# Performance work log

Hardware: AMD Instinct MI355X
Metric: run time of the kernel (lower is better)

## Reference

```python
import jax, jax.numpy as jnp
import numpy as np

B, NQ, NK = 4, 2048, 2048
D_MODEL, H, DK, DV, M = 512, 8, 64, 64, 40


def setup_inputs() -> dict:
    key = jax.random.key(0)
    ks = jax.random.split(key, 12)
    s = 0.02  # param init scale (stand-in for xavier)
    return {
        "queries": jax.random.normal(ks[0], (B, NQ, D_MODEL), jnp.float32),
        "keys": jax.random.normal(ks[1], (B, NK, D_MODEL), jnp.float32),
        "values": jax.random.normal(ks[2], (B, NK, D_MODEL), jnp.float32),
        "attention_weights": jax.random.uniform(ks[3], (B, H, NQ, NK), jnp.float32),
        "attention_mask": jax.random.randint(ks[4], (B, H, NQ, NK), 0, 2) == 1,
        "Wq": jax.random.normal(ks[5], (D_MODEL, H * DK), jnp.float32) * s,
        "bq": jnp.zeros((H * DK,), jnp.float32),
        "Wk": jax.random.normal(ks[6], (D_MODEL, H * DK), jnp.float32) * s,
        "bk": jnp.zeros((H * DK,), jnp.float32),
        "Wv": jax.random.normal(ks[7], (D_MODEL, H * DV), jnp.float32) * s,
        "bv": jnp.zeros((H * DV,), jnp.float32),
        "Wo": jax.random.normal(ks[8], (H * DV, D_MODEL), jnp.float32) * s,
        "bo": jnp.zeros((D_MODEL,), jnp.float32),
        "m_k": jax.random.normal(ks[9], (1, M, H * DK), jnp.float32) * s,
        "m_v": jax.random.normal(ks[10], (1, M, H * DV), jnp.float32) * s,
    }


def reference(queries, keys, values, attention_weights, attention_mask,
              Wq, bq, Wk, bk, Wv, bv, Wo, bo, m_k, m_v):
    b, nq, _ = queries.shape
    nk = keys.shape[1]
    # learned memory slots, scaled and broadcast over batch
    mk = jnp.sqrt(jnp.float32(DK)) * jnp.broadcast_to(m_k, (b, M, H * DK))
    mv = jnp.sqrt(jnp.float32(M)) * jnp.broadcast_to(m_v, (b, M, H * DV))
    q = (queries @ Wq + bq).reshape(b, nq, H, DK).transpose(0, 2, 1, 3)      # (b,h,nq,dk)
    k = jnp.concatenate([keys @ Wk + bk, mk], axis=1)
    k = k.reshape(b, nk + M, H, DK).transpose(0, 2, 3, 1)                     # (b,h,dk,nk+m)
    v = jnp.concatenate([values @ Wv + bv, mv], axis=1)
    v = v.reshape(b, nk + M, H, DV).transpose(0, 2, 1, 3)                     # (b,h,nk+m,dv)
    att = jnp.matmul(q, k) / jnp.sqrt(jnp.float32(DK))                        # (b,h,nq,nk+m)
    att_x = att[..., :nk] * attention_weights
    att_x = jnp.where(attention_mask, -jnp.inf, att_x)
    att = jnp.concatenate([att_x, att[..., nk:]], axis=-1)
    att = jax.nn.softmax(att, axis=-1)
    out = jnp.matmul(att, v).transpose(0, 2, 1, 3).reshape(b, nq, H * DV)
    return out @ Wo + bo
```

## Files before the change

kernel.cpp:

```cpp
#include <hip/hip_runtime.h>
#include <hip/hip_bf16.h>
#include <cstdint>
#include <cstddef>

typedef __bf16 bf16_t;
typedef __bf16 bf16x8 __attribute__((ext_vector_type(8)));
typedef __bf16 bf16x4 __attribute__((ext_vector_type(4)));
typedef float  f32x4  __attribute__((ext_vector_type(4)));

#define B_    4
#define NQ_   2048
#define NK_   2048
#define H_    8
#define MSL_  40
#define NKP_  2112
#define SCL2  0.18033688011112042f

#define GLOAD_LDS16(GP, LP)                                                        \
    __builtin_amdgcn_global_load_lds(                                              \
        (const __attribute__((address_space(1))) unsigned int*)(GP),               \
        (__attribute__((address_space(3))) unsigned int*)(LP), 16, 0, 0)

__global__ void detect_mask(const unsigned int* __restrict__ m, int* __restrict__ flag)
{
    __shared__ int found;
    if (threadIdx.x == 0) found = 0;
    __syncthreads();
    unsigned int acc = 0;
    for (int i = threadIdx.x; i < 65536; i += 256)
        acc |= (m[i] & 0xFFFFFF00u);
    if (acc) found = 1;
    __syncthreads();
    if (threadIdx.x == 0) *flag = found;
}

__global__ void transpose_convert4(const float* __restrict__ s0, const float* __restrict__ s1,
                                   const float* __restrict__ s2, const float* __restrict__ s3,
                                   bf16_t* __restrict__ d0, bf16_t* __restrict__ d1,
                                   bf16_t* __restrict__ d2, bf16_t* __restrict__ d3)
{
    const float* src; bf16_t* dst;
    switch (blockIdx.z) {
        case 0:  src = s0; dst = d0; break;
        case 1:  src = s1; dst = d1; break;
        case 2:  src = s2; dst = d2; break;
        default: src = s3; dst = d3; break;
    }
    __shared__ float t[32][33];
    int x  = blockIdx.x * 32 + threadIdx.x;
    int y0 = blockIdx.y * 32 + threadIdx.y;
#pragma unroll
    for (int i = 0; i < 32; i += 8)
        t[threadIdx.y + i][threadIdx.x] = src[(size_t)(y0 + i) * 512 + x];
    __syncthreads();
    int ox  = blockIdx.y * 32 + threadIdx.x;
    int oy0 = blockIdx.x * 32 + threadIdx.y;
#pragma unroll
    for (int i = 0; i < 32; i += 8)
        dst[(size_t)(oy0 + i) * 512 + ox] = (bf16_t)t[threadIdx.x][threadIdx.y + i];
}

__global__ void memfill(const float* __restrict__ m_k, const float* __restrict__ m_v,
                        bf16_t* __restrict__ Kbf, bf16_t* __restrict__ Vt)
{
    int tid = blockIdx.x * 256 + threadIdx.x;
    if (tid < 4 * 64 * 512) {
        int c  = tid & 511;
        int mi = (tid >> 9) & 63;
        int b  = tid >> 15;
        float v = (mi < MSL_) ? 8.0f * m_k[mi * 512 + c] : 0.0f;
        Kbf[((size_t)b * NKP_ + NK_ + mi) * 512 + c] = (bf16_t)v;
    } else {
        int t  = tid - 4 * 64 * 512;
        int mi = t & 63;
        int dv = (t >> 6) & 63;
        int h  = (t >> 12) & 7;
        int b  = t >> 15;
        float v = (mi < MSL_) ? 6.324555320336759f * m_v[mi * 512 + h * 64 + dv] : 0.0f;
        Vt[(((size_t)b * H_ + h) * 64 + dv) * NKP_ + NK_ + mi] = (bf16_t)v;
    }
}

template<bool AF32>
__device__ __forceinline__ void gemm_core(
    bf16_t (*As)[72], bf16_t (*Bs)[72],
    const void* __restrict__ Av, const bf16_t* __restrict__ BT,
    const float* __restrict__ bias, void* __restrict__ dstv,
    int dstBS, int epi, float scale)
{
    const int tid = threadIdx.x;
    const int w = tid >> 6, l = tid & 63, lg = l >> 4, lr = l & 15;
    const int wr = w >> 1, wc = w & 1;
    const int blockM = blockIdx.x * 128, blockN = blockIdx.y * 128;

    f32x4 acc[4][4];
    const f32x4 zv = {0.f, 0.f, 0.f, 0.f};
#pragma unroll
    for (int i = 0; i < 4; i++)
#pragma unroll
        for (int j = 0; j < 4; j++) acc[i][j] = zv;

    const int ar = tid >> 1;
    const int ac = (tid & 1) * 32;

    for (int k0 = 0; k0 < 512; k0 += 64) {
        if (k0) __syncthreads();
        if constexpr (AF32) {
            const float* arow = (const float*)Av + (size_t)(blockM + ar) * 512 + k0 + ac;
#pragma unroll
            for (int i = 0; i < 8; i++) {
                float4 v = ((const float4*)arow)[i];
                bf16x4 pk = {(bf16_t)v.x, (bf16_t)v.y, (bf16_t)v.z, (bf16_t)v.w};
                *(bf16x4*)&As[ar][ac + i * 4] = pk;
            }
        } else {
            const bf16_t* arow = (const bf16_t*)Av + (size_t)(blockM + ar) * 512 + k0 + ac;
#pragma unroll
            for (int i = 0; i < 4; i++)
                *(uint4*)&As[ar][ac + i * 8] = ((const uint4*)arow)[i];
        }
        {
            const bf16_t* brow = BT + (size_t)(blockN + ar) * 512 + k0 + ac;
#pragma unroll
            for (int i = 0; i < 4; i++)
                *(uint4*)&Bs[ar][ac + i * 8] = ((const uint4*)brow)[i];
        }
        __syncthreads();
#pragma unroll
        for (int ks = 0; ks < 2; ks++) {
            bf16x8 af[4], bfr[4];
#pragma unroll
            for (int mi = 0; mi < 4; mi++)
                af[mi] = *(const bf16x8*)&As[wr * 64 + mi * 16 + lr][ks * 32 + lg * 8];
#pragma unroll
            for (int ni = 0; ni < 4; ni++)
                bfr[ni] = *(const bf16x8*)&Bs[wc * 64 + ni * 16 + lr][ks * 32 + lg * 8];
#pragma unroll
            for (int mi = 0; mi < 4; mi++)
#pragma unroll
                for (int ni = 0; ni < 4; ni++)
                    acc[mi][ni] = __builtin_amdgcn_mfma_f32_16x16x32_bf16(af[mi], bfr[ni], acc[mi][ni], 0, 0, 0);
        }
    }

    const int colbase = blockN + wc * 64;
    float bias_v[4];
#pragma unroll
    for (int ni = 0; ni < 4; ni++) bias_v[ni] = bias[colbase + ni * 16 + lr];

#pragma unroll
    for (int mi = 0; mi < 4; mi++) {
        const int r0 = blockM + wr * 64 + mi * 16 + lg * 4;
#pragma unroll
        for (int ni = 0; ni < 4; ni++) {
            const int c = colbase + ni * 16 + lr;
            f32x4 v = acc[mi][ni];
            if (epi == 2) {
                float* dst = (float*)dstv;
#pragma unroll
                for (int j = 0; j < 4; j++)
                    dst[(size_t)(r0 + j) * 512 + c] = (v[j] + bias_v[ni]) * scale;
            } else if (epi == 0) {
                bf16_t* dst = (bf16_t*)dstv;
#pragma unroll
                for (int j = 0; j < 4; j++) {
                    int rr = r0 + j;
                    int bb = rr >> 11, nn = rr & 2047;
                    dst[((size_t)bb * dstBS + nn) * 512 + c] = (bf16_t)((v[j] + bias_v[ni]) * scale);
                }
            } else {
                bf16_t* dst = (bf16_t*)dstv;
                int bb = r0 >> 11, n0 = r0 & 2047;
                int hh = c >> 6, dv = c & 63;
                bf16x4 pk;
#pragma unroll
                for (int j = 0; j < 4; j++) pk[j] = (bf16_t)((v[j] + bias_v[ni]) * scale);
                *(bf16x4*)(dst + (((size_t)bb * H_ + hh) * 64 + dv) * NKP_ + n0) = pk;
            }
        }
    }
}

__global__ __launch_bounds__(256) void gemm_qkv(
    const float* __restrict__ q, const float* __restrict__ k, const float* __restrict__ v,
    const bf16_t* __restrict__ WqT, const bf16_t* __restrict__ WkT, const bf16_t* __restrict__ WvT,
    const float* __restrict__ bq, const float* __restrict__ bk, const float* __restrict__ bv,
    bf16_t* __restrict__ Qbf, bf16_t* __restrict__ Kbf, bf16_t* __restrict__ Vt)
{
    __shared__ bf16_t As[128][72];
    __shared__ bf16_t Bs[128][72];
    const void* Av; const bf16_t* BT; const float* bias; void* dst;
    int dstBS, epi; float scale = 1.0f;
    switch (blockIdx.z) {
        case 0:  Av = q; BT = WqT; bias = bq; dst = Qbf; dstBS = 2048; epi = 0; scale = SCL2; break;
        case 1:  Av = k; BT = WkT; bias = bk; dst = Kbf; dstBS = NKP_; epi = 0; break;
        default: Av = v; BT = WvT; bias = bv; dst = Vt;  dstBS = 0;    epi = 1; break;
    }
    gemm_core<true>(As, Bs, Av, BT, bias, dst, dstBS, epi, scale);
}

__global__ __launch_bounds__(256) void gemm_fin(
    const bf16_t* __restrict__ Obuf, const bf16_t* __restrict__ WoT,
    const float* __restrict__ bo, float* __restrict__ out)
{
    __shared__ bf16_t As[128][72];
    __shared__ bf16_t Bs[128][72];
    gemm_core<false>(As, Bs, Obuf, WoT, bo, out, 0, 2, 1.0f);
}

template<bool BYTEM>
__global__ __launch_bounds__(512) void attn_fused(
    const bf16_t* __restrict__ Qbf, const bf16_t* __restrict__ Kbf,
    const bf16_t* __restrict__ Vt, const float* __restrict__ attw,
    const void* __restrict__ maskv, const int* __restrict__ mflag,
    bf16_t* __restrict__ Obuf)
{
    if ((*mflag != 0) != BYTEM) return;

    __shared__ bf16_t Ks[2][64][64];
    __shared__ bf16_t Vs[2][64][64];
    __shared__ bf16_t Pl[8][1024];

    const int tid = threadIdx.x;
    const int wv = tid >> 6, l = tid & 63, lg = l >> 4, lr = l & 15;
    const int qt = blockIdx.x, h = blockIdx.y, b = blockIdx.z;
    const int q0w = qt * 128 + wv * 16;
    bf16_t* Pw = &Pl[wv][0];

    const size_t bh = (size_t)(b * H_ + h);
    const float* wbase = attw + bh * (size_t)NQ_ * NK_;
    const unsigned char* mb8 = (const unsigned char*)maskv + bh * (size_t)NQ_ * NK_;
    const int* mb32 = (const int*)maskv + bh * (size_t)NQ_ * NK_;
    const char* kbase8 = (const char*)(Kbf + (size_t)b * NKP_ * 512 + h * 64);
    const char* vbase8 = (const char*)(Vt + bh * 64 * (size_t)NKP_);

    bf16x8 qf0 = *(const bf16x8*)&Qbf[((size_t)b * NQ_ + q0w + lr) * 512 + h * 64 + lg * 8];
    bf16x8 qf1 = *(const bf16x8*)&Qbf[((size_t)b * NQ_ + q0w + lr) * 512 + h * 64 + 32 + lg * 8];

    const f32x4 zv = {0.f, 0.f, 0.f, 0.f};
    f32x4 oacc[4];
#pragma unroll
    for (int i = 0; i < 4; i++) oacc[i] = zv;
    float lsum = 0.f;
    f32x4 sA[4];

    f32x4 wA[4], wB[4];
    unsigned mA[4], mB[4];
    unsigned miA[16], miB[16];

    const int srow = l >> 3;
    const int scsw = ((l & 7) ^ (srow & 7)) * 16;

#define STAGE(BUF, KCB) do {                                                      \
    const int r_ = wv * 8 + srow;                                                 \
    GLOAD_LDS16(kbase8 + (size_t)((KCB) + r_) * 1024 + scsw,                      \
                (char*)&Ks[BUF][0][0] + wv * 1024);                               \
    GLOAD_LDS16(vbase8 + (size_t)r_ * 4224 + (size_t)(KCB) * 2 + scsw,            \
                (char*)&Vs[BUF][0][0] + wv * 1024);                               \
} while (0)

#define PREFETCH(KT, WB_, MB_, MIB_) do {                                         \
    const float* wp_ = wbase + (size_t)(q0w + lr) * NK_ + (KT) * 64 + lg * 4;     \
    _Pragma("unroll") for (int n_ = 0; n_ < 4; n_++)                              \
        WB_[n_] = *(const f32x4*)(wp_ + n_ * 16);                                 \
    if constexpr (BYTEM) {                                                        \
        const unsigned char* mp_ = mb8 + (size_t)(q0w + lr) * NK_ + (KT) * 64 + lg * 4; \
        _Pragma("unroll") for (int n_ = 0; n_ < 4; n_++)                          \
            MB_[n_] = *(const unsigned*)(mp_ + n_ * 16);                          \
    } else {                                                                      \
        const int* mp_ = mb32 + (size_t)(q0w + lr) * NK_ + (KT) * 64 + lg * 4;    \
        _Pragma("unroll") for (int n_ = 0; n_ < 4; n_++) {                        \
            uint4 t_ = *(const uint4*)(mp_ + n_ * 16);                            \
            MIB_[n_ * 4 + 0] = t_.x; MIB_[n_ * 4 + 1] = t_.y;                     \
            MIB_[n_ * 4 + 2] = t_.z; MIB_[n_ * 4 + 3] = t_.w; }                   \
    }                                                                             \
} while (0)

#define QKT_LDS(BC) do {                                                          \
    const int sw_ = (lg ^ (lr & 7)) * 8;                                          \
    _Pragma("unroll") for (int n_ = 0; n_ < 4; n_++) {                            \
        const int kr_ = n_ * 16 + lr;                                             \
        f32x4 a_ = zv;                                                            \
        a_ = __builtin_amdgcn_mfma_f32_16x16x32_bf16(*(const bf16x8*)&Ks[BC][kr_][sw_], qf0, a_, 0, 0, 0); \
        a_ = __builtin_amdgcn_mfma_f32_16x16x32_bf16(*(const bf16x8*)&Ks[BC][kr_][sw_ ^ 32], qf1, a_, 0, 0, 0); \
        sA[n_] = a_;                                                              \
    }                                                                             \
} while (0)

#define APPLY(WB_, MB_, MIB_) do {                                                \
    _Pragma("unroll") for (int n_ = 0; n_ < 4; n_++)                              \
    _Pragma("unroll") for (int j_ = 0; j_ < 4; j_++) {                            \
        bool mk_;                                                                 \
        if constexpr (BYTEM) mk_ = ((MB_[n_] >> (8 * j_)) & 0xffu) != 0;          \
        else                 mk_ = (MIB_[n_ * 4 + j_] != 0);                      \
        sA[n_][j_] = mk_ ? -1e30f : sA[n_][j_] * WB_[n_][j_];                     \
    }                                                                             \
} while (0)

#define SMPV(BC) do {                                                             \
    _Pragma("unroll") for (int n_ = 0; n_ < 4; n_++)                              \
    _Pragma("unroll") for (int j_ = 0; j_ < 4; j_++) {                            \
        float p_ = exp2f(sA[n_][j_]);                                             \
        sA[n_][j_] = p_; lsum += p_;                                              \
    }                                                                             \
    _Pragma("unroll") for (int n_ = 0; n_ < 4; n_++) {                            \
        int c_ = n_ * 2 + (lg >> 1);                                              \
        int qp_ = (lr + 4 * c_) & 15;                                             \
        bf16x4 pk_ = {(bf16_t)sA[n_][0], (bf16_t)sA[n_][1],                       \
                      (bf16_t)sA[n_][2], (bf16_t)sA[n_][3]};                      \
        *(bf16x4*)&Pw[c_ * 128 + qp_ * 8 + (lg & 1) * 4] = pk_;                   \
    }                                                                             \
    bf16x8 pf0_ = *(const bf16x8*)&Pw[lg * 128 + ((lr + 4 * lg) & 15) * 8];       \
    bf16x8 pf1_ = *(const bf16x8*)&Pw[(4 + lg) * 128 + ((lr + 4 * (4 + lg)) & 15) * 8]; \
    const int vsw_ = (lg ^ (lr & 7)) * 8;                                         \
    _Pragma("unroll") for (int n2_ = 0; n2_ < 4; n2_++) {                         \
        const int vr_ = n2_ * 16 + lr;                                            \
        oacc[n2_] = __builtin_amdgcn_mfma_f32_16x16x32_bf16(*(const bf16x8*)&Vs[BC][vr_][vsw_], pf0_, oacc[n2_], 0, 0, 0); \
        oacc[n2_] = __builtin_amdgcn_mfma_f32_16x16x32_bf16(*(const bf16x8*)&Vs[BC][vr_][vsw_ ^ 32], pf1_, oacc[n2_], 0, 0, 0); \
    }                                                                             \
} while (0)

#define WAITBAR(WCNT) do {                                                        \
    asm volatile("s_waitcnt vmcnt(" WCNT ")" ::: "memory");                       \
    __builtin_amdgcn_s_barrier();                                                 \
    __builtin_amdgcn_sched_barrier(0);                                            \
} while (0)

#define BODY(KT, BC, BN, WC_, MC_, MIC_) do {                                     \
    WAITBAR("8");                                                                 \
    if ((KT) < 31) { STAGE(BN, ((KT) + 1) * 64); }                                \
    __builtin_amdgcn_sched_barrier(0);                                            \
    QKT_LDS(BC);                                                                  \
    APPLY(WC_, MC_, MIC_);                                                        \
    if ((KT) < 30) { PREFETCH((KT) + 2, WC_, MC_, MIC_); }                        \
    SMPV(BC);                                                                     \
} while (0)

    STAGE(0, 2048);
    __builtin_amdgcn_sched_barrier(0);
    PREFETCH(0, wA, mA, miA);

    {
        WAITBAR("8");
        STAGE(1, 0);
        __builtin_amdgcn_sched_barrier(0);
        QKT_LDS(0);
#pragma unroll
        for (int n_ = 0; n_ < 4; n_++)
#pragma unroll
            for (int j_ = 0; j_ < 4; j_++) {
                int kloc = n_ * 16 + lg * 4 + j_;
                sA[n_][j_] = (kloc >= MSL_) ? -1e30f : sA[n_][j_];
            }
        PREFETCH(1, wB, mB, miB);
        SMPV(0);
    }

    for (int kt = 0; kt < 30; kt += 2) {
        BODY(kt,     1, 0, wA, mA, miA);
        BODY(kt + 1, 0, 1, wB, mB, miB);
    }
    BODY(30, 1, 0, wA, mA, miA);
    {
        WAITBAR("0");
        QKT_LDS(0);
        APPLY(wB, mB, miB);
        SMPV(0);
    }

    float ts = lsum;
    ts += __shfl_xor(ts, 16);
    ts += __shfl_xor(ts, 32);
    float invl = 1.0f / ts;
#pragma unroll
    for (int n2 = 0; n2 < 4; n2++) {
        bf16x4 ov = {(bf16_t)(oacc[n2][0] * invl), (bf16_t)(oacc[n2][1] * invl),
                     (bf16_t)(oacc[n2][2] * invl), (bf16_t)(oacc[n2][3] * invl)};
        *(bf16x4*)&Obuf[((size_t)b * NQ_ + q0w + lr) * 512 + h * 64 + n2 * 16 + lg * 4] = ov;
    }

#undef STAGE
#undef PREFETCH
#undef QKT_LDS
#undef APPLY
#undef SMPV
#undef WAITBAR
#undef BODY
}

extern "C" void kernel_launch(void* const* d_in, const int* in_sizes, int n_in,
                              void* d_out, int out_size, void* d_ws, size_t ws_size,
                              hipStream_t stream)
{
    const float* queries = (const float*)d_in[0];
    const float* keys    = (const float*)d_in[1];
    const float* values  = (const float*)d_in[2];
    const float* attw    = (const float*)d_in[3];
    const void*  maskv   = d_in[4];
    const float* Wq = (const float*)d_in[5];
    const float* bq = (const float*)d_in[6];
    const float* Wk = (const float*)d_in[7];
    const float* bk = (const float*)d_in[8];
    const float* Wv = (const float*)d_in[9];
    const float* bv = (const float*)d_in[10];
    const float* Wo = (const float*)d_in[11];
    const float* bo = (const float*)d_in[12];
    const float* m_k = (const float*)d_in[13];
    const float* m_v = (const float*)d_in[14];

    char* ws = (char*)d_ws;
    bf16_t* WqT  = (bf16_t*)(ws + 0);
    bf16_t* WkT  = (bf16_t*)(ws + 524288);
    bf16_t* WvT  = (bf16_t*)(ws + 1048576);
    bf16_t* WoT  = (bf16_t*)(ws + 1572864);
    bf16_t* Qbf  = (bf16_t*)(ws + 2097152);
    bf16_t* Kbf  = (bf16_t*)(ws + 10485760);
    bf16_t* Vt   = (bf16_t*)(ws + 19136512);
    bf16_t* Obuf = (bf16_t*)(ws + 27787264);
    int*    mflag = (int*)(ws + 36175872);

    detect_mask<<<1, 256, 0, stream>>>((const unsigned int*)maskv, mflag);
    transpose_convert4<<<dim3(16, 16, 4), dim3(32, 8), 0, stream>>>(
        Wq, Wk, Wv, Wo, WqT, WkT, WvT, WoT);
    memfill<<<1024, 256, 0, stream>>>(m_k, m_v, Kbf, Vt);

    gemm_qkv<<<dim3(64, 4, 3), 256, 0, stream>>>(
        queries, keys, values, WqT, WkT, WvT, bq, bk, bv, Qbf, Kbf, Vt);

    attn_fused<true><<<dim3(16, H_, B_), 512, 0, stream>>>(Qbf, Kbf, Vt, attw, maskv, mflag, Obuf);
    attn_fused<false><<<dim3(16, H_, B_), 512, 0, stream>>>(Qbf, Kbf, Vt, attw, maskv, mflag, Obuf);

    gemm_fin<<<dim3(64, 4), 256, 0, stream>>>(Obuf, WoT, bo, (float*)d_out);
    (void)in_sizes; (void)n_in; (void)out_size; (void)ws_size;
}
```

Measured before the change: 395.9 us.

## Split key tile across wave halves in attention and reduce partials via LDS

Each attention block now covers 64 query rows instead of 128. The eight waves split into two groups, and each group handles half of every 64-key tile. The partial output accumulators and row sums are merged through shared memory at the end, and the grid doubles to 32 query tiles. The aim is more blocks and smaller per-wave register state, which should give better occupancy and latency hiding on the bandwidth-bound weight and mask stream. In exchange, every block loads K/V tiles for half as many queries, which doubles K/V staging traffic, and the merge adds two barriers plus an LDS reduction.

```diff
diff --git a/kernel.cpp b/kernel.cpp
--- a/kernel.cpp
+++ b/kernel.cpp
@@ -219,12 +219,14 @@
 
     __shared__ bf16_t Ks[2][64][64];
     __shared__ bf16_t Vs[2][64][64];
-    __shared__ bf16_t Pl[8][1024];
+    __shared__ bf16_t Pl[8][512];
 
     const int tid = threadIdx.x;
     const int wv = tid >> 6, l = tid & 63, lg = l >> 4, lr = l & 15;
+    const int hk = wv >> 2;
+    const int kofs = hk * 32;
     const int qt = blockIdx.x, h = blockIdx.y, b = blockIdx.z;
-    const int q0w = qt * 128 + wv * 16;
+    const int q0w = qt * 64 + (wv & 3) * 16;
     bf16_t* Pw = &Pl[wv][0];
 
     const size_t bh = (size_t)(b * H_ + h);
@@ -242,11 +244,11 @@
 #pragma unroll
     for (int i = 0; i < 4; i++) oacc[i] = zv;
     float lsum = 0.f;
-    f32x4 sA[4];
-
-    f32x4 wA[4], wB[4];
-    unsigned mA[4], mB[4];
-    unsigned miA[16], miB[16];
+    f32x4 sA[2];
+
+    f32x4 wA[2], wB[2];
+    unsigned mA[2], mB[2];
+    unsigned miA[8], miB[8];
 
     const int srow = l >> 3;
     const int scsw = ((l & 7) ^ (srow & 7)) * 16;
@@ -260,26 +262,26 @@
 } while (0)
 
 #define PREFETCH(KT, WB_, MB_, MIB_) do {                                         \
-    const float* wp_ = wbase + (size_t)(q0w + lr) * NK_ + (KT) * 64 + lg * 4;     \
-    _Pragma("unroll") for (int n_ = 0; n_ < 4; n_++)                              \
-        WB_[n_] = *(const f32x4*)(wp_ + n_ * 16);                                 \
+    const float* wp_ = wbase + (size_t)(q0w + lr) * NK_ + (KT) * 64 + kofs + lg * 4; \
+    WB_[0] = *(const f32x4*)(wp_);                                                \
+    WB_[1] = *(const f32x4*)(wp_ + 16);                                           \
     if constexpr (BYTEM) {                                                        \
-        const unsigned char* mp_ = mb8 + (size_t)(q0w + lr) * NK_ + (KT) * 64 + lg * 4; \
-        _Pragma("unroll") for (int n_ = 0; n_ < 4; n_++)                          \
-            MB_[n_] = *(const unsigned*)(mp_ + n_ * 16);                          \
+        const unsigned char* mp_ = mb8 + (size_t)(q0w + lr) * NK_ + (KT) * 64 + kofs + lg * 4; \
+        MB_[0] = *(const unsigned*)(mp_);                                         \
+        MB_[1] = *(const unsigned*)(mp_ + 16);                                    \
     } else {                                                                      \
-        const int* mp_ = mb32 + (size_t)(q0w + lr) * NK_ + (KT) * 64 + lg * 4;    \
-        _Pragma("unroll") for (int n_ = 0; n_ < 4; n_++) {                        \
-            uint4 t_ = *(const uint4*)(mp_ + n_ * 16);                            \
-            MIB_[n_ * 4 + 0] = t_.x; MIB_[n_ * 4 + 1] = t_.y;                     \
-            MIB_[n_ * 4 + 2] = t_.z; MIB_[n_ * 4 + 3] = t_.w; }                   \
+        const int* mp_ = mb32 + (size_t)(q0w + lr) * NK_ + (KT) * 64 + kofs + lg * 4; \
+        uint4 t0_ = *(const uint4*)(mp_);                                         \
+        uint4 t1_ = *(const uint4*)(mp_ + 16);                                    \
+        MIB_[0]=t0_.x; MIB_[1]=t0_.y; MIB_[2]=t0_.z; MIB_[3]=t0_.w;               \
+        MIB_[4]=t1_.x; MIB_[5]=t1_.y; MIB_[6]=t1_.z; MIB_[7]=t1_.w;               \
     }                                                                             \
 } while (0)
 
 #define QKT_LDS(BC) do {                                                          \
     const int sw_ = (lg ^ (lr & 7)) * 8;                                          \
-    _Pragma("unroll") for (int n_ = 0; n_ < 4; n_++) {                            \
-        const int kr_ = n_ * 16 + lr;                                             \
+    _Pragma("unroll") for (int n_ = 0; n_ < 2; n_++) {                            \
+        const int kr_ = kofs + n_ * 16 + lr;                                      \
         f32x4 a_ = zv;                                                            \
         a_ = __builtin_amdgcn_mfma_f32_16x16x32_bf16(*(const bf16x8*)&Ks[BC][kr_][sw_], qf0, a_, 0, 0, 0); \
         a_ = __builtin_amdgcn_mfma_f32_16x16x32_bf16(*(const bf16x8*)&Ks[BC][kr_][sw_ ^ 32], qf1, a_, 0, 0, 0); \
@@ -288,7 +290,7 @@
 } while (0)
 
 #define APPLY(WB_, MB_, MIB_) do {                                                \
-    _Pragma("unroll") for (int n_ = 0; n_ < 4; n_++)                              \
+    _Pragma("unroll") for (int n_ = 0; n_ < 2; n_++)                              \
     _Pragma("unroll") for (int j_ = 0; j_ < 4; j_++) {                            \
         bool mk_;                                                                 \
         if constexpr (BYTEM) mk_ = ((MB_[n_] >> (8 * j_)) & 0xffu) != 0;          \
@@ -298,12 +300,12 @@
 } while (0)
 
 #define SMPV(BC) do {                                                             \
-    _Pragma("unroll") for (int n_ = 0; n_ < 4; n_++)                              \
+    _Pragma("unroll") for (int n_ = 0; n_ < 2; n_++)                              \
     _Pragma("unroll") for (int j_ = 0; j_ < 4; j_++) {                            \
         float p_ = exp2f(sA[n_][j_]);                                             \
         sA[n_][j_] = p_; lsum += p_;                                              \
     }                                                                             \
-    _Pragma("unroll") for (int n_ = 0; n_ < 4; n_++) {                            \
+    _Pragma("unroll") for (int n_ = 0; n_ < 2; n_++) {                            \
         int c_ = n_ * 2 + (lg >> 1);                                              \
         int qp_ = (lr + 4 * c_) & 15;                                             \
         bf16x4 pk_ = {(bf16_t)sA[n_][0], (bf16_t)sA[n_][1],                       \
@@ -311,12 +313,10 @@
         *(bf16x4*)&Pw[c_ * 128 + qp_ * 8 + (lg & 1) * 4] = pk_;                   \
     }                                                                             \
     bf16x8 pf0_ = *(const bf16x8*)&Pw[lg * 128 + ((lr + 4 * lg) & 15) * 8];       \
-    bf16x8 pf1_ = *(const bf16x8*)&Pw[(4 + lg) * 128 + ((lr + 4 * (4 + lg)) & 15) * 8]; \
-    const int vsw_ = (lg ^ (lr & 7)) * 8;                                         \
     _Pragma("unroll") for (int n2_ = 0; n2_ < 4; n2_++) {                         \
         const int vr_ = n2_ * 16 + lr;                                            \
+        const int vsw_ = (((hk << 2) | lg) ^ (lr & 7)) * 8;                       \
         oacc[n2_] = __builtin_amdgcn_mfma_f32_16x16x32_bf16(*(const bf16x8*)&Vs[BC][vr_][vsw_], pf0_, oacc[n2_], 0, 0, 0); \
-        oacc[n2_] = __builtin_amdgcn_mfma_f32_16x16x32_bf16(*(const bf16x8*)&Vs[BC][vr_][vsw_ ^ 32], pf1_, oacc[n2_], 0, 0, 0); \
     }                                                                             \
 } while (0)
 
@@ -327,7 +327,7 @@
 } while (0)
 
 #define BODY(KT, BC, BN, WC_, MC_, MIC_) do {                                     \
-    WAITBAR("8");                                                                 \
+    WAITBAR("4");                                                                 \
     if ((KT) < 31) { STAGE(BN, ((KT) + 1) * 64); }                                \
     __builtin_amdgcn_sched_barrier(0);                                            \
     QKT_LDS(BC);                                                                  \
@@ -341,15 +341,15 @@
     PREFETCH(0, wA, mA, miA);
 
     {
-        WAITBAR("8");
+        WAITBAR("4");
         STAGE(1, 0);
         __builtin_amdgcn_sched_barrier(0);
         QKT_LDS(0);
 #pragma unroll
-        for (int n_ = 0; n_ < 4; n_++)
+        for (int n_ = 0; n_ < 2; n_++)
 #pragma unroll
             for (int j_ = 0; j_ < 4; j_++) {
-                int kloc = n_ * 16 + lg * 4 + j_;
+                int kloc = kofs + n_ * 16 + lg * 4 + j_;
                 sA[n_][j_] = (kloc >= MSL_) ? -1e30f : sA[n_][j_];
             }
         PREFETCH(1, wB, mB, miB);
@@ -368,15 +368,31 @@
         SMPV(0);
     }
 
-    float ts = lsum;
-    ts += __shfl_xor(ts, 16);
-    ts += __shfl_xor(ts, 32);
-    float invl = 1.0f / ts;
-#pragma unroll
-    for (int n2 = 0; n2 < 4; n2++) {
-        bf16x4 ov = {(bf16_t)(oacc[n2][0] * invl), (bf16_t)(oacc[n2][1] * invl),
-                     (bf16_t)(oacc[n2][2] * invl), (bf16_t)(oacc[n2][3] * invl)};
-        *(bf16x4*)&Obuf[((size_t)b * NQ_ + q0w + lr) * 512 + h * 64 + n2 * 16 + lg * 4] = ov;
+    __syncthreads();
+    if (hk) {
+        float* po = (float*)&Ks[0][0][0] + (wv - 4) * 1024;
+#pragma unroll
+        for (int n2 = 0; n2 < 4; n2++)
+            *(f32x4*)(po + l * 16 + n2 * 4) = oacc[n2];
+        ((float*)&Vs[0][0][0])[(wv - 4) * 64 + l] = lsum;
+    }
+    __syncthreads();
+    if (!hk) {
+        const float* po = (const float*)&Ks[0][0][0] + wv * 1024;
+#pragma unroll
+        for (int n2 = 0; n2 < 4; n2++)
+            oacc[n2] += *(const f32x4*)(po + l * 16 + n2 * 4);
+        lsum += ((const float*)&Vs[0][0][0])[wv * 64 + l];
+        float ts = lsum;
+        ts += __shfl_xor(ts, 16);
+        ts += __shfl_xor(ts, 32);
+        float invl = 1.0f / ts;
+#pragma unroll
+        for (int n2 = 0; n2 < 4; n2++) {
+            bf16x4 ov = {(bf16_t)(oacc[n2][0] * invl), (bf16_t)(oacc[n2][1] * invl),
+                         (bf16_t)(oacc[n2][2] * invl), (bf16_t)(oacc[n2][3] * invl)};
+            *(bf16x4*)&Obuf[((size_t)b * NQ_ + q0w + lr) * 512 + h * 64 + n2 * 16 + lg * 4] = ov;
+        }
     }
 
 #undef STAGE
@@ -427,8 +443,8 @@
     gemm_qkv<<<dim3(64, 4, 3), 256, 0, stream>>>(
         queries, keys, values, WqT, WkT, WvT, bq, bk, bv, Qbf, Kbf, Vt);
 
-    attn_fused<true><<<dim3(16, H_, B_), 512, 0, stream>>>(Qbf, Kbf, Vt, attw, maskv, mflag, Obuf);
-    attn_fused<false><<<dim3(16, H_, B_), 512, 0, stream>>>(Qbf, Kbf, Vt, attw, maskv, mflag, Obuf);
+    attn_fused<true><<<dim3(32, H_, B_), 512, 0, stream>>>(Qbf, Kbf, Vt, attw, maskv, mflag, Obuf);
+    attn_fused<false><<<dim3(32, H_, B_), 512, 0, stream>>>(Qbf, Kbf, Vt, attw, maskv, mflag, Obuf);
 
     gemm_fin<<<dim3(64, 4), 256, 0, stream>>>(Obuf, WoT, bo, (float*)d_out);
     (void)in_sizes; (void)n_in; (void)out_size; (void)ws_size;
```

New measurement: 373.1 us. 1.06x faster.

## Halve attention block to 4 waves and simplify pipeline to single-ahead prefetch with syncthreads

Applied to the files above, without the earlier changes.

The attention kernel now runs 256-thread blocks of 4 waves covering 64 query rows, with twice as many blocks, and each wave stages two K/V slices. The hand-tuned vmcnt wait plus raw barrier scheme is replaced by plain __syncthreads, and the attention-weight and mask prefetch now runs one tile ahead instead of two. The aim is more resident blocks and better latency hiding across blocks. In exchange, each block reuses its K/V tiles across fewer queries, K/V traffic doubles, and the global-load wait is now left to the compiler.

```diff
diff --git a/kernel.cpp b/kernel.cpp
--- a/kernel.cpp
+++ b/kernel.cpp
@@ -209,7 +209,7 @@
 }
 
 template<bool BYTEM>
-__global__ __launch_bounds__(512) void attn_fused(
+__global__ __launch_bounds__(256) void attn_fused(
     const bf16_t* __restrict__ Qbf, const bf16_t* __restrict__ Kbf,
     const bf16_t* __restrict__ Vt, const float* __restrict__ attw,
     const void* __restrict__ maskv, const int* __restrict__ mflag,
@@ -219,12 +219,12 @@
 
     __shared__ bf16_t Ks[2][64][64];
     __shared__ bf16_t Vs[2][64][64];
-    __shared__ bf16_t Pl[8][1024];
+    __shared__ bf16_t Pl[4][1024];
 
     const int tid = threadIdx.x;
     const int wv = tid >> 6, l = tid & 63, lg = l >> 4, lr = l & 15;
     const int qt = blockIdx.x, h = blockIdx.y, b = blockIdx.z;
-    const int q0w = qt * 128 + wv * 16;
+    const int q0w = qt * 64 + wv * 16;
     bf16_t* Pw = &Pl[wv][0];
 
     const size_t bh = (size_t)(b * H_ + h);
@@ -252,11 +252,14 @@
     const int scsw = ((l & 7) ^ (srow & 7)) * 16;
 
 #define STAGE(BUF, KCB) do {                                                      \
-    const int r_ = wv * 8 + srow;                                                 \
-    GLOAD_LDS16(kbase8 + (size_t)((KCB) + r_) * 1024 + scsw,                      \
-                (char*)&Ks[BUF][0][0] + wv * 1024);                               \
-    GLOAD_LDS16(vbase8 + (size_t)r_ * 4224 + (size_t)(KCB) * 2 + scsw,            \
-                (char*)&Vs[BUF][0][0] + wv * 1024);                               \
+    _Pragma("unroll") for (int pi_ = 0; pi_ < 2; pi_++) {                         \
+        const int p_ = wv * 2 + pi_;                                              \
+        const int r_ = p_ * 8 + srow;                                             \
+        GLOAD_LDS16(kbase8 + (size_t)((KCB) + r_) * 1024 + scsw,                  \
+                    (char*)&Ks[BUF][0][0] + p_ * 1024);                           \
+        GLOAD_LDS16(vbase8 + (size_t)r_ * 4224 + (size_t)(KCB) * 2 + scsw,        \
+                    (char*)&Vs[BUF][0][0] + p_ * 1024);                           \
+    }                                                                             \
 } while (0)
 
 #define PREFETCH(KT, WB_, MB_, MIB_) do {                                         \
@@ -320,30 +323,21 @@
     }                                                                             \
 } while (0)
 
-#define WAITBAR(WCNT) do {                                                        \
-    asm volatile("s_waitcnt vmcnt(" WCNT ")" ::: "memory");                       \
-    __builtin_amdgcn_s_barrier();                                                 \
-    __builtin_amdgcn_sched_barrier(0);                                            \
-} while (0)
-
-#define BODY(KT, BC, BN, WC_, MC_, MIC_) do {                                     \
-    WAITBAR("8");                                                                 \
-    if ((KT) < 31) { STAGE(BN, ((KT) + 1) * 64); }                                \
-    __builtin_amdgcn_sched_barrier(0);                                            \
+#define BODYT(KT, BC, BN, WB_, MB_, MIB_, WN_, MN_, MIN_) do {                    \
+    if ((KT) < 31) STAGE(BN, ((KT) + 1) * 64);                                    \
     QKT_LDS(BC);                                                                  \
-    APPLY(WC_, MC_, MIC_);                                                        \
-    if ((KT) < 30) { PREFETCH((KT) + 2, WC_, MC_, MIC_); }                        \
+    if ((KT) < 31) PREFETCH((KT) + 1, WN_, MN_, MIN_);                            \
+    APPLY(WB_, MB_, MIB_);                                                        \
     SMPV(BC);                                                                     \
+    __syncthreads();                                                              \
 } while (0)
 
     STAGE(0, 2048);
-    __builtin_amdgcn_sched_barrier(0);
     PREFETCH(0, wA, mA, miA);
+    __syncthreads();
 
     {
-        WAITBAR("8");
         STAGE(1, 0);
-        __builtin_amdgcn_sched_barrier(0);
         QKT_LDS(0);
 #pragma unroll
         for (int n_ = 0; n_ < 4; n_++)
@@ -352,20 +346,13 @@
                 int kloc = n_ * 16 + lg * 4 + j_;
                 sA[n_][j_] = (kloc >= MSL_) ? -1e30f : sA[n_][j_];
             }
-        PREFETCH(1, wB, mB, miB);
         SMPV(0);
-    }
-
-    for (int kt = 0; kt < 30; kt += 2) {
-        BODY(kt,     1, 0, wA, mA, miA);
-        BODY(kt + 1, 0, 1, wB, mB, miB);
-    }
-    BODY(30, 1, 0, wA, mA, miA);
-    {
-        WAITBAR("0");
-        QKT_LDS(0);
-        APPLY(wB, mB, miB);
-        SMPV(0);
+        __syncthreads();
+    }
+
+    for (int kt = 0; kt < 32; kt += 2) {
+        BODYT(kt,     1, 0, wA, mA, miA, wB, mB, miB);
+        BODYT(kt + 1, 0, 1, wB, mB, miB, wA, mA, miA);
     }
 
     float ts = lsum;
@@ -384,8 +371,7 @@
 #undef QKT_LDS
 #undef APPLY
 #undef SMPV
-#undef WAITBAR
-#undef BODY
+#undef BODYT
 }
 
 extern "C" void kernel_launch(void* const* d_in, const int* in_sizes, int n_in,
@@ -427,8 +413,8 @@
     gemm_qkv<<<dim3(64, 4, 3), 256, 0, stream>>>(
         queries, keys, values, WqT, WkT, WvT, bq, bk, bv, Qbf, Kbf, Vt);
 
-    attn_fused<true><<<dim3(16, H_, B_), 512, 0, stream>>>(Qbf, Kbf, Vt, attw, maskv, mflag, Obuf);
-    attn_fused<false><<<dim3(16, H_, B_), 512, 0, stream>>>(Qbf, Kbf, Vt, attw, maskv, mflag, Obuf);
+    attn_fused<true><<<dim3(32, H_, B_), 256, 0, stream>>>(Qbf, Kbf, Vt, attw, maskv, mflag, Obuf);
+    attn_fused<false><<<dim3(32, H_, B_), 256, 0, stream>>>(Qbf, Kbf, Vt, attw, maskv, mflag, Obuf);
 
     gemm_fin<<<dim3(64, 4), 256, 0, stream>>>(Obuf, WoT, bo, (float*)d_out);
     (void)in_sizes; (void)n_in; (void)out_size; (void)ws_size;
```

Measured after the change: 394.9 us. About the same (-0.3%).

## Deepen K/V LDS staging to four buffers and halve barriers per tile pair

Applied to the files above, without the earlier changes.

K and V shared-memory tiles go from double to quadruple buffering. The loop is restructured into periods that stage two future tiles at once, process two key tiles, then issue one __syncthreads. The explicit vmcnt waits plus barriers per tile are replaced by a single block-wide sync every two tiles, which aims to cut synchronisation overhead and give more prefetch slack. This doubles the K/V LDS footprint, which may reduce occupancy. __syncthreads may also wait for all outstanding memory ops, including the attention-weight prefetches, which could serialize loads.

```diff
diff --git a/kernel.cpp b/kernel.cpp
--- a/kernel.cpp
+++ b/kernel.cpp
@@ -217,8 +217,8 @@
 {
     if ((*mflag != 0) != BYTEM) return;
 
-    __shared__ bf16_t Ks[2][64][64];
-    __shared__ bf16_t Vs[2][64][64];
+    __shared__ bf16_t Ks[4][64][64];
+    __shared__ bf16_t Vs[4][64][64];
     __shared__ bf16_t Pl[8][1024];
 
     const int tid = threadIdx.x;
@@ -320,30 +320,28 @@
     }                                                                             \
 } while (0)
 
-#define WAITBAR(WCNT) do {                                                        \
-    asm volatile("s_waitcnt vmcnt(" WCNT ")" ::: "memory");                       \
-    __builtin_amdgcn_s_barrier();                                                 \
-    __builtin_amdgcn_sched_barrier(0);                                            \
-} while (0)
-
-#define BODY(KT, BC, BN, WC_, MC_, MIC_) do {                                     \
-    WAITBAR("8");                                                                 \
-    if ((KT) < 31) { STAGE(BN, ((KT) + 1) * 64); }                                \
-    __builtin_amdgcn_sched_barrier(0);                                            \
+#define SUBB(T, BC, W_, M_, MI_) do {                                            \
     QKT_LDS(BC);                                                                  \
-    APPLY(WC_, MC_, MIC_);                                                        \
-    if ((KT) < 30) { PREFETCH((KT) + 2, WC_, MC_, MIC_); }                        \
+    APPLY(W_, M_, MI_);                                                           \
+    if ((T) < 30) PREFETCH((T) + 2, W_, M_, MI_);                                 \
     SMPV(BC);                                                                     \
 } while (0)
 
+#define PERIOD(T, B0, B1, S0, S1) do {                                            \
+    if ((T) + 2 < 32) STAGE(S0, ((T) + 2) * 64);                                  \
+    if ((T) + 3 < 32) STAGE(S1, ((T) + 3) * 64);                                  \
+    SUBB((T),     B0, wA, mA, miA);                                               \
+    SUBB((T) + 1, B1, wB, mB, miB);                                               \
+    __syncthreads();                                                              \
+} while (0)
+
     STAGE(0, 2048);
-    __builtin_amdgcn_sched_barrier(0);
+    STAGE(1, 0);
+    STAGE(2, 64);
     PREFETCH(0, wA, mA, miA);
+    __syncthreads();
 
     {
-        WAITBAR("8");
-        STAGE(1, 0);
-        __builtin_amdgcn_sched_barrier(0);
         QKT_LDS(0);
 #pragma unroll
         for (int n_ = 0; n_ < 4; n_++)
@@ -354,19 +352,16 @@
             }
         PREFETCH(1, wB, mB, miB);
         SMPV(0);
-    }
-
-    for (int kt = 0; kt < 30; kt += 2) {
-        BODY(kt,     1, 0, wA, mA, miA);
-        BODY(kt + 1, 0, 1, wB, mB, miB);
-    }
-    BODY(30, 1, 0, wA, mA, miA);
-    {
-        WAITBAR("0");
-        QKT_LDS(0);
-        APPLY(wB, mB, miB);
-        SMPV(0);
-    }
+        __syncthreads();
+    }
+
+    for (int t = 0; t < 28; t += 4) {
+        PERIOD(t,     1, 2, 3, 0);
+        PERIOD(t + 2, 3, 0, 1, 2);
+    }
+    PERIOD(28, 1, 2, 3, 0);
+    SUBB(30, 3, wA, mA, miA);
+    SUBB(31, 0, wB, mB, miB);
 
     float ts = lsum;
     ts += __shfl_xor(ts, 16);
@@ -384,8 +379,8 @@
 #undef QKT_LDS
 #undef APPLY
 #undef SMPV
-#undef WAITBAR
-#undef BODY
+#undef SUBB
+#undef PERIOD
 }
 
 extern "C" void kernel_launch(void* const* d_in, const int* in_sizes, int n_in,
```

Result: faster. 336.5 us (-15.0%).
